# Kernel optimization log

Hardware: AMD Instinct MI355X
Metric: run time of the kernel (lower is better)

Reference implementation:

```python
import jax, jax.numpy as jnp
import numpy as np

B, T, I, O = 64, 1024, 512, 512
EPS = 1e-5


def setup_inputs() -> dict:
    key = jax.random.key(0)
    k1, k2 = jax.random.split(key)
    x = jax.random.normal(k1, (B, T, I), dtype=jnp.float32)
    W = jax.random.normal(k2, (4 * O, I + O), dtype=jnp.float32) * 0.02
    gamma = jnp.ones((4, O), dtype=jnp.float32)
    beta = jnp.zeros((4, O), dtype=jnp.float32)
    init_hx = jnp.zeros((1, O), dtype=jnp.float32)
    init_cx = jnp.zeros((1, O), dtype=jnp.float32)
    return {"x": x, "W": W, "gamma": gamma, "beta": beta,
            "init_hx": init_hx, "init_cx": init_cx}


def reference(x, W, gamma, beta, init_hx, init_cx):
    b = x.shape[0]
    o = init_hx.shape[-1]

    def step(carry, xt):
        h, c = carry
        # fused gate projection: [B, I+O] @ [I+O, 4O] -> [B, 4, O]
        z = jnp.concatenate([xt, h], axis=-1) @ W.T
        z = z.reshape(b, 4, o)
        # LayerNorm over the last TWO dims (gate axis + feature axis), per torch nn.LayerNorm([4, O])
        mu = jnp.mean(z, axis=(-2, -1), keepdims=True)
        var = jnp.var(z, axis=(-2, -1), keepdims=True)
        zn = (z - mu) * jax.lax.rsqrt(var + EPS) * gamma + beta
        gates = jax.nn.sigmoid(zn[:, :3])  # f, i, o gates
        f_g, i_g, o_g = gates[:, 0], gates[:, 1], gates[:, 2]
        h_state = jax.nn.gelu(zn[:, 3], approximate=False)  # dropout = identity (eval)
        c_new = f_g * c + i_g * h_state
        h_new = o_g * c_new
        return (h_new, c_new), h_new

    h0 = jnp.broadcast_to(init_hx, (b, o))
    c0 = jnp.broadcast_to(init_cx, (b, o))
    x_t = jnp.swapaxes(x, 0, 1)  # [T, B, I]
    _, hs = jax.lax.scan(step, (h0, c0), x_t)
    return jnp.swapaxes(hs, 0, 1)  # [B, T, O]
```

## Files before the change

kernel.cpp:

```cpp
#include <hip/hip_runtime.h>
#include <math.h>

#define B_  64
#define T_  1024
#define I_  512
#define O_  512
#define NZ  2048
#define KW  1024
#define EPS 1e-5f

#define SREC 32
#define NPROD 1024
#define OSL  16
#define BAILOUT (1u << 18)

typedef short bf8_t  __attribute__((ext_vector_type(8)));
typedef float f32x4  __attribute__((ext_vector_type(4)));
typedef unsigned uint4v __attribute__((ext_vector_type(4)));

__device__ __forceinline__ unsigned short f2bf(float f) {
  union { float f; unsigned u; } v; v.f = f;
  unsigned r = v.u + 0x7FFFu + ((v.u >> 16) & 1u);
  return (unsigned short)(r >> 16);
}
__device__ __forceinline__ float bf2f(unsigned short b) {
  union { unsigned u; float f; } v; v.u = ((unsigned)b) << 16;
  return v.f;
}

__global__ __launch_bounds__(256) void init_all(
    const float* __restrict__ init_hx,
    unsigned short* __restrict__ h, unsigned* __restrict__ sync) {
  int idx = blockIdx.x * 256 + threadIdx.x;
  if (idx < 2048) sync[idx] = 0u;
  if (idx < B_ * O_) h[idx] = f2bf(init_hx[idx & (O_ - 1)]);
}

__global__ __launch_bounds__(256) void wx_bf16(
    const float* __restrict__ W, unsigned short* __restrict__ Wbf) {
  int idx = blockIdx.x * 256 + threadIdx.x;
  int n  = idx >> 7;
  int k4 = (idx & 127) * 4;
  float4 v = *(const float4*)(W + (size_t)n * KW + k4);
  unsigned short* d = Wbf + (size_t)n * 512 + k4;
  d[0] = f2bf(v.x); d[1] = f2bf(v.y); d[2] = f2bf(v.z); d[3] = f2bf(v.w);
}

__global__ __launch_bounds__(256) void fused_rec(
    const float* __restrict__ x, const unsigned short* __restrict__ Wbf,
    const float* __restrict__ W, const float* __restrict__ gamma,
    const float* __restrict__ beta, const float* __restrict__ init_cx,
    unsigned short* __restrict__ zx, unsigned short* __restrict__ h,
    unsigned long long* __restrict__ part8, float* __restrict__ out,
    unsigned* __restrict__ flags) {

  __shared__ unsigned short smem[37888];

  const int tid  = threadIdx.x;
  const int w    = tid >> 6;
  const int lane = tid & 63;
  const int q    = lane >> 4;
  const int col  = lane & 15;
  unsigned* zxcnt = flags + 1024;

  if (blockIdx.x >= SREC) {
    const int p  = blockIdx.x - SREC;
    const int b  = p & 63;
    const int tc = p >> 6;
    const int m0 = b * T_ + tc * 64;

    unsigned short* xl  = smem;
    unsigned short* cst = smem + 33280;

    for (int e4 = tid; e4 < 64 * 128; e4 += 256) {
      int r  = e4 >> 7;
      int k4 = (e4 & 127) * 4;
      float4 v = *(const float4*)(x + (size_t)(m0 + r) * I_ + k4);
      unsigned short* d = &xl[r * 520 + k4];
      d[0] = f2bf(v.x); d[1] = f2bf(v.y); d[2] = f2bf(v.z); d[3] = f2bf(v.w);
    }
    __syncthreads();

    const unsigned short* arow = &xl[(16 * w + col) * 520];
    const int crow = tid >> 2;
    const int cc0  = (tid & 3) * 16;

    for (int nblk = 0; nblk < 32; ++nblk) {
      const int n0 = nblk * 64;
      f32x4 acc[4];
      #pragma unroll
      for (int i = 0; i < 4; ++i) acc[i] = (f32x4){0.f, 0.f, 0.f, 0.f};

      #pragma unroll
      for (int ks = 0; ks < 16; ++ks) {
        const int k0 = ks * 32 + q * 8;
        bf8_t af = *(const bf8_t*)(arow + k0);
        #pragma unroll
        for (int nt = 0; nt < 4; ++nt) {
          bf8_t bfr = *(const bf8_t*)(Wbf + (size_t)(n0 + nt * 16 + col) * 512 + k0);
          acc[nt] = __builtin_amdgcn_mfma_f32_16x16x32_bf16(af, bfr, acc[nt], 0, 0, 0);
        }
      }
      __syncthreads();
      #pragma unroll
      for (int nt = 0; nt < 4; ++nt)
        #pragma unroll
        for (int r = 0; r < 4; ++r)
          cst[(16 * w + 4 * q + r) * 72 + nt * 16 + col] = f2bf(acc[nt][r]);
      __syncthreads();
      {
        union { uint4v v; unsigned long long u[2]; } a0, a1;
        const uint4v* srcp = (const uint4v*)&cst[crow * 72 + cc0];
        a0.v = srcp[0]; a1.v = srcp[1];
        unsigned long long* dst =
            (unsigned long long*)&zx[(size_t)(m0 + crow) * NZ + n0 + cc0];
        __hip_atomic_store(dst + 0, a0.u[0], __ATOMIC_RELAXED, __HIP_MEMORY_SCOPE_AGENT);
        __hip_atomic_store(dst + 1, a0.u[1], __ATOMIC_RELAXED, __HIP_MEMORY_SCOPE_AGENT);
        __hip_atomic_store(dst + 2, a1.u[0], __ATOMIC_RELAXED, __HIP_MEMORY_SCOPE_AGENT);
        __hip_atomic_store(dst + 3, a1.u[1], __ATOMIC_RELAXED, __HIP_MEMORY_SCOPE_AGENT);
      }
    }
    __syncthreads();
    if (tid == 0)
      __hip_atomic_fetch_add(&zxcnt[tc], 1u, __ATOMIC_RELAXED,
                             __HIP_MEMORY_SCOPE_AGENT);
    return;
  }

  unsigned short* whlds = smem;
  const int s = blockIdx.x;
  const int o = s * OSL + col;

  for (int e4 = tid; e4 < 64 * 128; e4 += 256) {
    int r  = e4 >> 7;
    int k4 = (e4 & 127) * 4;
    int g  = r >> 4, np = r & 15;
    const float4 v =
        *(const float4*)(W + (size_t)(512 * g + OSL * s + np) * KW + I_ + k4);
    unsigned short* d = &whlds[r * 520 + k4];
    d[0] = f2bf(v.x); d[1] = f2bf(v.y); d[2] = f2bf(v.z); d[3] = f2bf(v.w);
  }

  float gma[4], bta[4], c_reg[4];
  #pragma unroll
  for (int g = 0; g < 4; ++g) { gma[g] = gamma[g * O_ + o]; bta[g] = beta[g * O_ + o]; }
  { float c0 = init_cx[o];
    #pragma unroll
    for (int r = 0; r < 4; ++r) c_reg[r] = c0; }

  {
    unsigned spins = 0;
    while (__hip_atomic_load(&zxcnt[0], __ATOMIC_RELAXED,
                             __HIP_MEMORY_SCOPE_AGENT) < 64u) {
      __builtin_amdgcn_s_sleep(2);
      if (++spins > BAILOUT) break;
    }
  }
  unsigned short zxl[16];
  #pragma unroll
  for (int g = 0; g < 4; ++g)
    #pragma unroll
    for (int r = 0; r < 4; ++r) {
      int b = 16 * w + 4 * q + r;
      zxl[g * 4 + r] = zx[((size_t)b * T_ + 0) * NZ + g * O_ + OSL * s + col];
    }

  __syncthreads();

  for (int t = 0; t < T_; ++t) {
    unsigned long long araw[32];
    const unsigned short* hrow = h + (16 * w + col) * O_;
    #pragma unroll
    for (int ks = 0; ks < 16; ++ks) {
      const unsigned long long* p =
          (const unsigned long long*)(hrow + ks * 32 + q * 8);
      araw[2 * ks]     = __hip_atomic_load(p,     __ATOMIC_RELAXED, __HIP_MEMORY_SCOPE_AGENT);
      araw[2 * ks + 1] = __hip_atomic_load(p + 1, __ATOMIC_RELAXED, __HIP_MEMORY_SCOPE_AGENT);
    }

    f32x4 acc[4];
    #pragma unroll
    for (int g = 0; g < 4; ++g) acc[g] = (f32x4){0.f, 0.f, 0.f, 0.f};

    #pragma unroll
    for (int ks = 0; ks < 16; ++ks) {
      union { unsigned long long u[2]; bf8_t v; } au;
      au.u[0] = araw[2 * ks]; au.u[1] = araw[2 * ks + 1];
      #pragma unroll
      for (int g = 0; g < 4; ++g) {
        bf8_t bfr = *(const bf8_t*)(&whlds[(g * 16 + col) * 520 + ks * 32 + q * 8]);
        acc[g] = __builtin_amdgcn_mfma_f32_16x16x32_bf16(au.v, bfr, acc[g], 0, 0, 0);
      }
    }

    float z[16];
    float s1[4], s2[4];
    #pragma unroll
    for (int r = 0; r < 4; ++r) { s1[r] = 0.f; s2[r] = 0.f; }
    #pragma unroll
    for (int g = 0; g < 4; ++g)
      #pragma unroll
      for (int r = 0; r < 4; ++r) {
        float zv = acc[g][r] + bf2f(zxl[g * 4 + r]);
        z[g * 4 + r] = zv;
        s1[r] += zv;
        s2[r] += zv * zv;
      }
    #pragma unroll
    for (int m = 1; m < 16; m <<= 1) {
      #pragma unroll
      for (int r = 0; r < 4; ++r) {
        s1[r] += __shfl_xor(s1[r], m, 64);
        s2[r] += __shfl_xor(s2[r], m, 64);
      }
    }
    if (col == 0) {
      #pragma unroll
      for (int r = 0; r < 4; ++r) {
        int b = 16 * w + 4 * q + r;
        union { float f[2]; unsigned long long u; } pv;
        pv.f[0] = s1[r]; pv.f[1] = s2[r];
        __hip_atomic_store(&part8[(size_t)s * 64 + b], pv.u,
                           __ATOMIC_RELAXED, __HIP_MEMORY_SCOPE_AGENT);
      }
    }

    __syncthreads();
    {
      const unsigned tgt = 2u * (unsigned)t + 1u;
      if (tid == 0)
        __hip_atomic_store(&flags[s * 16], tgt,
                           __ATOMIC_RELAXED, __HIP_MEMORY_SCOPE_AGENT);
      if (tid < 64) {
        const unsigned* fp = &flags[(lane & 31) * 16];
        while (__hip_atomic_load(fp, __ATOMIC_RELAXED, __HIP_MEMORY_SCOPE_AGENT) < tgt)
          __builtin_amdgcn_s_sleep(1);
      }
      __syncthreads();
    }

    float S1 = 0.f, S2 = 0.f;
    {
      const int brow = 16 * w + (lane & 15);
      const int sbase = (lane >> 4) * 8;
      #pragma unroll
      for (int i = 0; i < 8; ++i) {
        union { float f[2]; unsigned long long u; } pv;
        pv.u = __hip_atomic_load(&part8[(size_t)(sbase + i) * 64 + brow],
                                 __ATOMIC_RELAXED, __HIP_MEMORY_SCOPE_AGENT);
        S1 += pv.f[0]; S2 += pv.f[1];
      }
    }
    S1 += __shfl_xor(S1, 16, 64); S2 += __shfl_xor(S2, 16, 64);
    S1 += __shfl_xor(S1, 32, 64); S2 += __shfl_xor(S2, 32, 64);
    float mean_l = S1 * (1.f / NZ);
    float rstd_l = rsqrtf(S2 * (1.f / NZ) - mean_l * mean_l + EPS);

    float hnl[4];
    #pragma unroll
    for (int r = 0; r < 4; ++r) {
      int b = 16 * w + 4 * q + r;
      float mean = __shfl(mean_l, 4 * q + r, 64);
      float rstd = __shfl(rstd_l, 4 * q + r, 64);
      float zn0 = (z[0 * 4 + r] - mean) * rstd * gma[0] + bta[0];
      float zn1 = (z[1 * 4 + r] - mean) * rstd * gma[1] + bta[1];
      float zn2 = (z[2 * 4 + r] - mean) * rstd * gma[2] + bta[2];
      float zn3 = (z[3 * 4 + r] - mean) * rstd * gma[3] + bta[3];
      float fg = 1.f / (1.f + expf(-zn0));
      float ig = 1.f / (1.f + expf(-zn1));
      float og = 1.f / (1.f + expf(-zn2));
      float gg = 0.5f * zn3 * (1.f + erff(zn3 * 0.70710678118654752f));
      float cn = fg * c_reg[r] + ig * gg;
      float hn = og * cn;
      c_reg[r] = cn;
      hnl[r] = hn;
      __hip_atomic_store(&h[b * O_ + o], f2bf(hn),
                         __ATOMIC_RELAXED, __HIP_MEMORY_SCOPE_AGENT);
    }

    if (t + 1 < T_) {
      __syncthreads();
      const unsigned tgt = 2u * (unsigned)t + 2u;
      if (tid == 0)
        __hip_atomic_store(&flags[s * 16], tgt,
                           __ATOMIC_RELAXED, __HIP_MEMORY_SCOPE_AGENT);
      #pragma unroll
      for (int r = 0; r < 4; ++r) {
        int b = 16 * w + 4 * q + r;
        out[((size_t)b * T_ + t) * O_ + o] = hnl[r];
      }
      if (((t + 1) & 63) == 0) {
        const int tc = (t + 1) >> 6;
        unsigned spins = 0;
        while (__hip_atomic_load(&zxcnt[tc], __ATOMIC_RELAXED,
                                 __HIP_MEMORY_SCOPE_AGENT) < 64u) {
          __builtin_amdgcn_s_sleep(2);
          if (++spins > BAILOUT) break;
        }
      }
      #pragma unroll
      for (int g = 0; g < 4; ++g)
        #pragma unroll
        for (int r = 0; r < 4; ++r) {
          int b = 16 * w + 4 * q + r;
          zxl[g * 4 + r] =
              zx[((size_t)b * T_ + (t + 1)) * NZ + g * O_ + OSL * s + col];
        }
      if (tid < 64) {
        const unsigned* fp = &flags[(lane & 31) * 16];
        while (__hip_atomic_load(fp, __ATOMIC_RELAXED, __HIP_MEMORY_SCOPE_AGENT) < tgt)
          __builtin_amdgcn_s_sleep(1);
      }
      __syncthreads();
    } else {
      #pragma unroll
      for (int r = 0; r < 4; ++r) {
        int b = 16 * w + 4 * q + r;
        out[((size_t)b * T_ + t) * O_ + o] = hnl[r];
      }
    }
  }
}

extern "C" void kernel_launch(void* const* d_in, const int* in_sizes, int n_in,
                              void* d_out, int out_size, void* d_ws, size_t ws_size,
                              hipStream_t stream) {
  const float* x       = (const float*)d_in[0];
  const float* W       = (const float*)d_in[1];
  const float* gamma   = (const float*)d_in[2];
  const float* beta    = (const float*)d_in[3];
  const float* init_hx = (const float*)d_in[4];
  const float* init_cx = (const float*)d_in[5];
  float* out = (float*)d_out;
  (void)in_sizes; (void)n_in; (void)out_size; (void)ws_size;

  char* ws = (char*)d_ws;
  unsigned*           flags = (unsigned*)(ws);
  unsigned long long* part8 = (unsigned long long*)(ws + 8192);
  unsigned short*     h     = (unsigned short*)(ws + 32768);
  unsigned short*     Wbf   = (unsigned short*)(ws + (1 << 20));
  unsigned short*     zx    = (unsigned short*)(ws + (4 << 20));

  init_all<<<128, 256, 0, stream>>>(init_hx, h, flags);
  wx_bf16<<<1024, 256, 0, stream>>>(W, Wbf);
  fused_rec<<<SREC + NPROD, 256, 0, stream>>>(x, Wbf, W, gamma, beta, init_cx,
                                              zx, h, part8, out, flags);
}
```

Before: 9.420 ms.

## Store input projections in a four-chunk ring buffer gated by recurrence progress

Replaces the full [B*T, 4O] bf16 zx buffer with a ring of four 64-step chunks. Producer blocks for later chunks now wait on a progress counter that recurrent block 0 publishes each step before they overwrite a slot. Reads of zx become 32-bit atomic loads with half-word extraction. The smaller footprint can stay resident in cache, at the cost of producers stalling on the serial recurrence and some extra per-step signalling.

After: 8.887 ms. 1.06x faster.

```diff
diff --git a/kernel.cpp b/kernel.cpp
--- a/kernel.cpp
+++ b/kernel.cpp
@@ -13,6 +13,7 @@
 #define NPROD 1024
 #define OSL  16
 #define BAILOUT (1u << 18)
+#define RING 4
 
 typedef short bf8_t  __attribute__((ext_vector_type(8)));
 typedef float f32x4  __attribute__((ext_vector_type(4)));
@@ -26,6 +27,9 @@
 __device__ __forceinline__ float bf2f(unsigned short b) {
   union { unsigned u; float f; } v; v.u = ((unsigned)b) << 16;
   return v.f;
+}
+__device__ __forceinline__ size_t zx_row(int b, int t) {
+  return (size_t)(((t >> 6) & (RING - 1)) * 64 + b) * 64 + (t & 63);
 }
 
 __global__ __launch_bounds__(256) void init_all(
@@ -61,13 +65,28 @@
   const int lane = tid & 63;
   const int q    = lane >> 4;
   const int col  = lane & 15;
-  unsigned* zxcnt = flags + 1024;
+  unsigned* zxcnt    = flags + 1024;
+  unsigned* progress = flags + 768;
 
   if (blockIdx.x >= SREC) {
-    const int p  = blockIdx.x - SREC;
-    const int b  = p & 63;
-    const int tc = p >> 6;
-    const int m0 = b * T_ + tc * 64;
+    const int p   = blockIdx.x - SREC;
+    const int b   = p & 63;
+    const int tc  = p >> 6;
+    const int m0x = b * T_ + tc * 64;
+    const int m0z = ((tc & (RING - 1)) * 64 + b) * 64;
+
+    if (tc >= RING) {
+      const unsigned gate = 2u * (unsigned)((tc - RING) * 64 + 63) + 1u;
+      if (tid == 0) {
+        unsigned spins = 0;
+        while (__hip_atomic_load(progress, __ATOMIC_RELAXED,
+                                 __HIP_MEMORY_SCOPE_AGENT) < gate) {
+          __builtin_amdgcn_s_sleep(64);
+          if (++spins > BAILOUT) break;
+        }
+      }
+      __syncthreads();
+    }
 
     unsigned short* xl  = smem;
     unsigned short* cst = smem + 33280;
@@ -75,7 +94,7 @@
     for (int e4 = tid; e4 < 64 * 128; e4 += 256) {
       int r  = e4 >> 7;
       int k4 = (e4 & 127) * 4;
-      float4 v = *(const float4*)(x + (size_t)(m0 + r) * I_ + k4);
+      float4 v = *(const float4*)(x + (size_t)(m0x + r) * I_ + k4);
       unsigned short* d = &xl[r * 520 + k4];
       d[0] = f2bf(v.x); d[1] = f2bf(v.y); d[2] = f2bf(v.z); d[3] = f2bf(v.w);
     }
@@ -113,7 +132,7 @@
         const uint4v* srcp = (const uint4v*)&cst[crow * 72 + cc0];
         a0.v = srcp[0]; a1.v = srcp[1];
         unsigned long long* dst =
-            (unsigned long long*)&zx[(size_t)(m0 + crow) * NZ + n0 + cc0];
+            (unsigned long long*)&zx[(size_t)(m0z + crow) * NZ + n0 + cc0];
         __hip_atomic_store(dst + 0, a0.u[0], __ATOMIC_RELAXED, __HIP_MEMORY_SCOPE_AGENT);
         __hip_atomic_store(dst + 1, a0.u[1], __ATOMIC_RELAXED, __HIP_MEMORY_SCOPE_AGENT);
         __hip_atomic_store(dst + 2, a1.u[0], __ATOMIC_RELAXED, __HIP_MEMORY_SCOPE_AGENT);
@@ -148,6 +167,9 @@
     #pragma unroll
     for (int r = 0; r < 4; ++r) c_reg[r] = c0; }
 
+  const int wsel = col & 1;
+  const int widx = col >> 1;
+
   {
     unsigned spins = 0;
     while (__hip_atomic_load(&zxcnt[0], __ATOMIC_RELAXED,
@@ -162,7 +184,11 @@
     #pragma unroll
     for (int r = 0; r < 4; ++r) {
       int b = 16 * w + 4 * q + r;
-      zxl[g * 4 + r] = zx[((size_t)b * T_ + 0) * NZ + g * O_ + OSL * s + col];
+      const unsigned* rowp =
+          (const unsigned*)(zx + zx_row(b, 0) * NZ + g * O_ + OSL * s);
+      unsigned vw = __hip_atomic_load(rowp + widx, __ATOMIC_RELAXED,
+                                      __HIP_MEMORY_SCOPE_AGENT);
+      zxl[g * 4 + r] = (unsigned short)(wsel ? (vw >> 16) : (vw & 0xffffu));
     }
 
   __syncthreads();
@@ -303,14 +329,20 @@
         #pragma unroll
         for (int r = 0; r < 4; ++r) {
           int b = 16 * w + 4 * q + r;
-          zxl[g * 4 + r] =
-              zx[((size_t)b * T_ + (t + 1)) * NZ + g * O_ + OSL * s + col];
+          const unsigned* rowp =
+              (const unsigned*)(zx + zx_row(b, t + 1) * NZ + g * O_ + OSL * s);
+          unsigned vw = __hip_atomic_load(rowp + widx, __ATOMIC_RELAXED,
+                                          __HIP_MEMORY_SCOPE_AGENT);
+          zxl[g * 4 + r] = (unsigned short)(wsel ? (vw >> 16) : (vw & 0xffffu));
         }
       if (tid < 64) {
         const unsigned* fp = &flags[(lane & 31) * 16];
         while (__hip_atomic_load(fp, __ATOMIC_RELAXED, __HIP_MEMORY_SCOPE_AGENT) < tgt)
           __builtin_amdgcn_s_sleep(1);
       }
+      if (s == 0 && tid == 0)
+        __hip_atomic_store(progress, tgt,
+                           __ATOMIC_RELAXED, __HIP_MEMORY_SCOPE_AGENT);
       __syncthreads();
     } else {
       #pragma unroll
```
